# Kernel optimization log

Measured on AMD Instinct MI355X. Metric: run time of the kernel, lower is better.

Reference implementation:

```python
import jax, jax.numpy as jnp
import numpy as np

DIM = 2048
H = 16
HD = DIM // H  # 128
EPS = 1e-6


def _rmsnorm(x, w):
    # x: [b, s, d] (float32 math, matches torch RMSNorm .float())
    return x * jax.lax.rsqrt(jnp.mean(x * x, axis=-1, keepdims=True) + EPS) * w


def _rope(x, freqs):
    # x: [b, s, d]; freqs: [s, HD//2, 2] (real, imag) -- complex multiply per pair
    b, s, d = x.shape
    xp = x.reshape(b, s, H, HD // 2, 2)
    xr, xi = xp[..., 0], xp[..., 1]
    fr = freqs[None, :, None, :, 0]
    fi = freqs[None, :, None, :, 1]
    out = jnp.stack([xr * fr - xi * fi, xr * fi + xi * fr], axis=-1)
    return out.reshape(b, s, d)


def _attn(q, k, v):
    # q: [b, sq, d], k/v: [b, skv, d] -> standard SDPA over H heads
    b, sq, d = q.shape
    skv = k.shape[1]
    qh = q.reshape(b, sq, H, HD)
    kh = k.reshape(b, skv, H, HD)
    vh = v.reshape(b, skv, H, HD)
    scores = jnp.einsum('bqhd,bkhd->bhqk', qh, kh) / np.sqrt(HD).astype(np.float32)
    p = jax.nn.softmax(scores, axis=-1)
    out = jnp.einsum('bhqk,bkhd->bqhd', p, vh)
    return out.reshape(b, sq, d)


def _linear(x, w, bias):
    # torch Linear convention: w [out, in]
    return jnp.einsum('bsi,oi->bso', x, w) + bias


def setup_inputs() -> dict:
    key = jax.random.key(0)
    ks = jax.random.split(key, 24)
    rn = lambda k, sh, s=1.0: jax.random.normal(k, sh, dtype=jnp.float32) * s
    B, SX, SC, SR = 2, 2048, 512, 512
    W = 0.02
    return {
        'x': rn(ks[0], (B, SX, DIM)),
        'cam_emb': rn(ks[1], (B, SC, DIM)),
        'render_emb': rn(ks[2], (B, SR, DIM)),
        'freqs_x': rn(ks[3], (SX, HD // 2, 2)),
        'freqs_cam': rn(ks[4], (SC, HD // 2, 2)),
        'freqs_render': rn(ks[5], (SR, HD // 2, 2)),
        'wq': rn(ks[6], (DIM, DIM), W), 'bq': jnp.zeros((DIM,), jnp.float32),
        'wk': rn(ks[7], (DIM, DIM), W), 'bk': jnp.zeros((DIM,), jnp.float32),
        'wv': rn(ks[8], (DIM, DIM), W), 'bv': jnp.zeros((DIM,), jnp.float32),
        'wkr': rn(ks[9], (DIM, DIM), W), 'bkr': jnp.zeros((DIM,), jnp.float32),
        'wvr': rn(ks[10], (DIM, DIM), W), 'bvr': jnp.zeros((DIM,), jnp.float32),
        'wo': rn(ks[11], (DIM, DIM), W), 'bo': jnp.zeros((DIM,), jnp.float32),
        'gq': jnp.ones((DIM,), jnp.float32),
        'gk': jnp.ones((DIM,), jnp.float32),
    }


def reference(x, cam_emb, render_emb, freqs_x, freqs_cam, freqs_render,
              wq, bq, wk, bk, wv, bv, wkr, bkr, wvr, bvr, wo, bo, gq, gk):
    q = _rope(_rmsnorm(_linear(x, wq, bq), gq), freqs_x)
    k_cam = _rope(_rmsnorm(_linear(cam_emb, wk, bk), gk), freqs_cam)
    k_ren = _rope(_rmsnorm(_linear(render_emb, wkr, bkr), gk), freqs_render)
    v_cam = _linear(cam_emb, wv, bv)
    v_ren = _linear(render_emb, wvr, bvr)
    k = jnp.concatenate([k_cam, k_ren], axis=1)
    v = jnp.concatenate([v_cam, v_ren], axis=1)
    out = _attn(q, k, v)
    return _linear(out, wo, bo)
```

## Files before the change

kernel.cpp:

```cpp
#include <hip/hip_runtime.h>

typedef short bf16x8 __attribute__((ext_vector_type(8)));
typedef float f32x4 __attribute__((ext_vector_type(4)));
typedef unsigned short ushort_t;
typedef unsigned int uint_t;

#define DIM 2048
#define NH 16
#define HD 128

__device__ __forceinline__ ushort_t f2b(float f) {
    union { float f; uint_t u; } a; a.f = f;
    uint_t u = a.u;
    return (ushort_t)((u + 0x7fffu + ((u >> 16) & 1u)) >> 16);
}

__device__ __forceinline__ float b2f(ushort_t s) {
    union { uint_t u; float f; } a; a.u = ((uint_t)s) << 16;
    return a.f;
}

__device__ __forceinline__ uint_t cvt_pk_bf16(float lo, float hi) {
    uint_t r;
    asm("v_cvt_pk_bf16_f32 %0, %1, %2" : "=v"(r) : "v"(lo), "v"(hi));
    return r;
}

__device__ __forceinline__ void gload_lds16(const void* g, void* l) {
    void* gg = const_cast<void*>(g);
    __builtin_amdgcn_global_load_lds(
        (__attribute__((address_space(1))) uint_t*)gg,
        (__attribute__((address_space(3))) uint_t*)l, 16, 0, 0);
}

struct CvtWArgs { const float* s[6]; };
__global__ __launch_bounds__(256) void k_cvtw(CvtWArgs a, ushort_t* __restrict__ dst) {
    int y = blockIdx.y;
    const float* in = a.s[y];
    ushort_t* out = dst + (size_t)y * 4194304;
    int idx = (blockIdx.x * 256 + threadIdx.x) * 8;
    float4 p = *(const float4*)(in + idx);
    float4 q = *(const float4*)(in + idx + 4);
    uint4 o;
    o.x = (uint_t)f2b(p.x) | ((uint_t)f2b(p.y) << 16);
    o.y = (uint_t)f2b(p.z) | ((uint_t)f2b(p.w) << 16);
    o.z = (uint_t)f2b(q.x) | ((uint_t)f2b(q.y) << 16);
    o.w = (uint_t)f2b(q.z) | ((uint_t)f2b(q.w) << 16);
    *(uint4*)(out + idx) = o;
}

struct Cvt3Args { const float* s[3]; ushort_t* d[3]; int n[3]; };
__global__ __launch_bounds__(256) void k_cvt3(Cvt3Args a) {
    int y = blockIdx.y;
    int idx = (blockIdx.x * 256 + threadIdx.x) * 8;
    if (idx >= a.n[y]) return;
    const float* in = a.s[y];
    ushort_t* out = a.d[y];
    float4 p = *(const float4*)(in + idx);
    float4 q = *(const float4*)(in + idx + 4);
    uint4 o;
    o.x = (uint_t)f2b(p.x) | ((uint_t)f2b(p.y) << 16);
    o.y = (uint_t)f2b(p.z) | ((uint_t)f2b(p.w) << 16);
    o.z = (uint_t)f2b(q.x) | ((uint_t)f2b(q.y) << 16);
    o.w = (uint_t)f2b(q.z) | ((uint_t)f2b(q.w) << 16);
    *(uint4*)(out + idx) = o;
}

struct G8 {
    const ushort_t* A;
    const ushort_t* B;
    const float* bias0;
    const float* bias1;
    void* out0;
    void* out1;
};

__global__ __launch_bounds__(512, 2) void k_g256(G8 p0, G8 p1, G8 p2) {
    extern __shared__ __align__(16) char sm[];
    int tid = threadIdx.x, lane = tid & 63, w = tid >> 6;
    int c = lane & 15, g = lane >> 4;
    int wr = w >> 2, wc = w & 3;

    int flat = blockIdx.x;
    G8 ar;
    int bm, bn, isKV = 0, kvoff = 0;
    {
        int re = (flat & 7) * 32 + (flat >> 3);
        if (re < 128) { ar = p0; bm = re & 15; bn = re >> 4; }
        else {
            int r2 = re - 128;
            int z = r2 >> 6; r2 &= 63;
            ar = z ? p2 : p1;
            bm = r2 & 3; bn = r2 >> 2;
            isKV = 1; kvoff = z ? 512 : 0;
        }
    }

    int wj0 = 2 * w, wj1 = 2 * w + 1;
    int l3 = lane >> 3;
    int swz = ((lane & 7) ^ l3) << 4;
    int RA0 = (wj0 >> 3) * 128 + (wj0 & 7) * 8 + l3;
    int RA1 = (wj1 >> 3) * 128 + (wj1 & 7) * 8 + l3;
    int LB0 = wj0 * 8 + l3;
    int LB1 = wj1 * 8 + l3;
    int RB0 = (LB0 >> 5) * 64 + (LB0 & 15) * 2 + ((LB0 >> 4) & 1);
    int RB1 = (LB1 >> 5) * 64 + (LB1 & 15) * 2 + ((LB1 >> 4) & 1);
    const char* sA0 = (const char*)ar.A + (size_t)(bm * 256 + RA0) * 4096 + swz;
    const char* sA1 = (const char*)ar.A + (size_t)(bm * 256 + RA1) * 4096 + swz;
    const char* sB0 = (const char*)ar.B + (size_t)(bn * 256 + RB0) * 4096 + swz;
    const char* sB1 = (const char*)ar.B + (size_t)(bn * 256 + RB1) * 4096 + swz;
    char* dA0 = sm + wj0 * 1024;
    char* dA1 = sm + wj1 * 1024;
    char* dB0 = sm + 32768 + wj0 * 1024;
    char* dB1 = sm + 32768 + wj1 * 1024;

    auto SA = [&](int buf, int half, int t) {
        gload_lds16(sA0 + (size_t)half * 262144 + t * 128, dA0 + buf + half * 16384);
        gload_lds16(sA1 + (size_t)half * 262144 + t * 128, dA1 + buf + half * 16384);
    };
    auto SB = [&](int buf, int half, int t) {
        gload_lds16(sB0 + (size_t)half * 131072 + t * 128, dB0 + buf + half * 16384);
        gload_lds16(sB1 + (size_t)half * 131072 + t * 128, dB1 + buf + half * 16384);
    };

    int bKS0 = (g << 4) ^ ((c & 7) << 4);
    int bKS1 = (64 | (g << 4)) ^ ((c & 7) << 4);
    int aoffL = wr * 8192 + c * 128;
    int boffL = 32768 + wc * 4096 + c * 128;

    f32x4 acc[8][4];
#pragma unroll
    for (int m = 0; m < 8; m++)
#pragma unroll
        for (int n = 0; n < 4; n++) acc[m][n] = (f32x4){0.f, 0.f, 0.f, 0.f};

    bf16x8 aF[4][2], bF0[2][2], bF1[2][2];

    auto RA = [&](int buf, int mh) {
#pragma unroll
        for (int m = 0; m < 4; m++) {
            aF[m][0] = *(const bf16x8*)(sm + buf + mh * 16384 + aoffL + m * 2048 + bKS0);
            aF[m][1] = *(const bf16x8*)(sm + buf + mh * 16384 + aoffL + m * 2048 + bKS1);
        }
    };
    auto RB = [&](int buf, int nh, bf16x8 (&bF)[2][2]) {
#pragma unroll
        for (int n = 0; n < 2; n++) {
            bF[n][0] = *(const bf16x8*)(sm + buf + boffL + nh * 16384 + n * 2048 + bKS0);
            bF[n][1] = *(const bf16x8*)(sm + buf + boffL + nh * 16384 + n * 2048 + bKS1);
        }
    };
    auto MF = [&](int mh, int nh, bf16x8 (&bF)[2][2]) {
        __builtin_amdgcn_s_setprio(1);
#pragma unroll
        for (int m = 0; m < 4; m++)
#pragma unroll
            for (int n = 0; n < 2; n++)
#pragma unroll
                for (int ks = 0; ks < 2; ks++)
                    acc[mh * 4 + m][nh * 2 + n] = __builtin_amdgcn_mfma_f32_16x16x32_bf16(
                        aF[m][ks], bF[n][ks], acc[mh * 4 + m][nh * 2 + n], 0, 0, 0);
        __builtin_amdgcn_s_setprio(0);
    };

    SA(0, 0, 0); SB(0, 0, 0); SA(0, 1, 0); SB(0, 1, 0);
    SA(65536, 0, 1); SB(65536, 0, 1);
    asm volatile("s_waitcnt vmcnt(8)" ::: "memory");
    __builtin_amdgcn_s_barrier();

#pragma unroll 1
    for (int i = 0; i < 16; ++i) {
        int Tb  = 2 * i + 1;
        int Ta2 = (2 * i + 2 > 31) ? 31 : 2 * i + 2;
        int Tb2 = (2 * i + 3 > 31) ? 31 : 2 * i + 3;
        RA(0, 0); RB(0, 0, bF0);
        SA(65536, 1, Tb);
        __builtin_amdgcn_s_barrier();
        MF(0, 0, bF0);
        asm volatile("s_waitcnt vmcnt(6)" ::: "memory");
        __builtin_amdgcn_s_barrier();
        RB(0, 1, bF1);
        SB(65536, 1, Tb);
        __builtin_amdgcn_s_barrier();
        MF(0, 1, bF1);
        __builtin_amdgcn_s_barrier();
        RA(0, 1);
        SA(0, 0, Ta2);
        __builtin_amdgcn_s_barrier();
        MF(1, 0, bF0);
        __builtin_amdgcn_s_barrier();
        SB(0, 0, Ta2);
        __builtin_amdgcn_s_barrier();
        MF(1, 1, bF1);
        asm volatile("s_waitcnt vmcnt(8)" ::: "memory");
        __builtin_amdgcn_s_barrier();
        RA(65536, 0); RB(65536, 0, bF0);
        SA(0, 1, Ta2);
        __builtin_amdgcn_s_barrier();
        MF(0, 0, bF0);
        asm volatile("s_waitcnt vmcnt(6)" ::: "memory");
        __builtin_amdgcn_s_barrier();
        RB(65536, 1, bF1);
        SB(0, 1, Ta2);
        __builtin_amdgcn_s_barrier();
        MF(0, 1, bF1);
        __builtin_amdgcn_s_barrier();
        RA(65536, 1);
        SA(65536, 0, Tb2);
        __builtin_amdgcn_s_barrier();
        MF(1, 0, bF0);
        __builtin_amdgcn_s_barrier();
        SB(65536, 0, Tb2);
        __builtin_amdgcn_s_barrier();
        MF(1, 1, bF1);
        asm volatile("s_waitcnt vmcnt(8)" ::: "memory");
        __builtin_amdgcn_s_barrier();
    }

    int orow0 = bm * 256 + wr * 128 + g * 4;
    int colb0 = bn * 256 + wc * 64 + c * 2;
    if (!isKV || bn < 8) {
        ushort_t* o0 = (ushort_t*)ar.out0;
#pragma unroll
        for (int nh = 0; nh < 2; nh++) {
            int colb = colb0 + nh * 32;
            float2 bv = *(const float2*)(ar.bias0 + colb);
#pragma unroll
            for (int m = 0; m < 8; m++)
#pragma unroll
                for (int q = 0; q < 4; q++) {
                    uint_t pk = cvt_pk_bf16(acc[m][nh * 2][q] + bv.x,
                                            acc[m][nh * 2 + 1][q] + bv.y);
                    *(uint_t*)(o0 + (size_t)(orow0 + m * 16 + q) * 2048 + colb) = pk;
                }
        }
    } else {
        ushort_t* o1 = (ushort_t*)ar.out1;
#pragma unroll
        for (int nh = 0; nh < 2; nh++)
#pragma unroll
            for (int np = 0; np < 2; np++) {
                int col2 = colb0 + nh * 32 + np - 2048;
                int h = col2 >> 7, d = col2 & 127;
                float bvs = ar.bias1[col2];
#pragma unroll
                for (int m = 0; m < 8; m++) {
                    int r = orow0 + m * 16;
                    int bb = r >> 9;
                    int kvg = kvoff + (r & 511);
                    int t = kvg >> 6, ki = kvg & 63;
                    uint2 wv;
                    wv.x = cvt_pk_bf16(acc[m][nh * 2 + np][0] + bvs, acc[m][nh * 2 + np][1] + bvs);
                    wv.y = cvt_pk_bf16(acc[m][nh * 2 + np][2] + bvs, acc[m][nh * 2 + np][3] + bvs);
                    *(uint2*)(o1 + (size_t)((bb * 16 + h) * 16 + t) * 8192 + d * 64 + ki) = wv;
                }
            }
    }
}

__global__ __launch_bounds__(512, 2) void k_g128(G8 p0) {
    extern __shared__ __align__(16) char sm[];
    int tid = threadIdx.x, lane = tid & 63, w = tid >> 6;
    int c = lane & 15, g = lane >> 4;
    int wr = w >> 2, wc = w & 3;

    int flat = blockIdx.x;
    int re = (flat & 7) * 32 + (flat >> 3);
    int bm = re & 31, bn = re >> 5;
    G8 ar = p0;

    int l3 = lane >> 3;
    int swz = ((lane & 7) ^ l3) << 4;
    int wj0 = 2 * w, wj1 = 2 * w + 1;
    int LB0 = wj0 * 8 + l3;
    int LB1 = wj1 * 8 + l3;
    int RB0 = (LB0 >> 5) * 64 + (LB0 & 15) * 2 + ((LB0 >> 4) & 1);
    int RB1 = (LB1 >> 5) * 64 + (LB1 & 15) * 2 + ((LB1 >> 4) & 1);
    const char* sA  = (const char*)ar.A + (size_t)(bm * 128 + w * 8 + l3) * 4096 + swz;
    const char* sB0 = (const char*)ar.B + (size_t)(bn * 256 + RB0) * 4096 + swz;
    const char* sB1 = (const char*)ar.B + (size_t)(bn * 256 + RB1) * 4096 + swz;
    char* dA  = sm + w * 1024;
    char* dB0 = sm + 16384 + wj0 * 1024;
    char* dB1 = sm + 16384 + wj1 * 1024;

    auto SA = [&](int buf, int half, int t) {
        gload_lds16(sA + (size_t)half * 262144 + t * 128, dA + buf + half * 8192);
    };
    auto SB = [&](int buf, int half, int t) {
        gload_lds16(sB0 + (size_t)half * 131072 + t * 128, dB0 + buf + half * 16384);
        gload_lds16(sB1 + (size_t)half * 131072 + t * 128, dB1 + buf + half * 16384);
    };

    int bKS0 = (g << 4) ^ ((c & 7) << 4);
    int bKS1 = (64 | (g << 4)) ^ ((c & 7) << 4);
    int aoffL = wr * 8192 + c * 128;
    int boffL = 16384 + wc * 4096 + c * 128;

    f32x4 acc[4][4];
#pragma unroll
    for (int m = 0; m < 4; m++)
#pragma unroll
        for (int n = 0; n < 4; n++) acc[m][n] = (f32x4){0.f, 0.f, 0.f, 0.f};

    bf16x8 aF[2][2], bF0[2][2], bF1[2][2];

    auto RA = [&](int buf, int mhp) {
#pragma unroll
        for (int m = 0; m < 2; m++) {
            aF[m][0] = *(const bf16x8*)(sm + buf + aoffL + (mhp * 2 + m) * 2048 + bKS0);
            aF[m][1] = *(const bf16x8*)(sm + buf + aoffL + (mhp * 2 + m) * 2048 + bKS1);
        }
    };
    auto RB = [&](int buf, int nh, bf16x8 (&bF)[2][2]) {
#pragma unroll
        for (int n = 0; n < 2; n++) {
            bF[n][0] = *(const bf16x8*)(sm + buf + boffL + nh * 16384 + n * 2048 + bKS0);
            bF[n][1] = *(const bf16x8*)(sm + buf + boffL + nh * 16384 + n * 2048 + bKS1);
        }
    };
    auto MF = [&](int mhp, int nh, bf16x8 (&bF)[2][2]) {
        __builtin_amdgcn_s_setprio(1);
#pragma unroll
        for (int m = 0; m < 2; m++)
#pragma unroll
            for (int n = 0; n < 2; n++)
#pragma unroll
                for (int ks = 0; ks < 2; ks++)
                    acc[mhp * 2 + m][nh * 2 + n] = __builtin_amdgcn_mfma_f32_16x16x32_bf16(
                        aF[m][ks], bF[n][ks], acc[mhp * 2 + m][nh * 2 + n], 0, 0, 0);
        __builtin_amdgcn_s_setprio(0);
    };

    const int B1 = 49152;
    SA(0, 0, 0); SA(0, 1, 0); SB(0, 0, 0); SB(0, 1, 0);
    SA(B1, 0, 1);
    asm volatile("s_waitcnt vmcnt(1)" ::: "memory");
    __builtin_amdgcn_s_barrier();

#pragma unroll 1
    for (int i = 0; i < 16; ++i) {
        int Tb  = 2 * i + 1;
        int Ta2 = (2 * i + 2 > 31) ? 31 : 2 * i + 2;
        int Tb2 = (2 * i + 3 > 31) ? 31 : 2 * i + 3;
        RA(0, 0); RB(0, 0, bF0);
        SA(B1, 1, Tb);
        __builtin_amdgcn_s_barrier();
        MF(0, 0, bF0);
        __builtin_amdgcn_s_barrier();
        RB(0, 1, bF1);
        SB(B1, 0, Tb);
        __builtin_amdgcn_s_barrier();
        MF(0, 1, bF1);
        __builtin_amdgcn_s_barrier();
        RA(0, 1);
        SB(B1, 1, Tb);
        __builtin_amdgcn_s_barrier();
        MF(1, 0, bF0);
        __builtin_amdgcn_s_barrier();
        SA(0, 0, Ta2);
        __builtin_amdgcn_s_barrier();
        MF(1, 1, bF1);
        asm volatile("s_waitcnt vmcnt(3)" ::: "memory");
        __builtin_amdgcn_s_barrier();
        RA(B1, 0); RB(B1, 0, bF0);
        SA(0, 1, Ta2);
        __builtin_amdgcn_s_barrier();
        MF(0, 0, bF0);
        asm volatile("s_waitcnt vmcnt(2)" ::: "memory");
        __builtin_amdgcn_s_barrier();
        RB(B1, 1, bF1);
        SB(0, 0, Ta2);
        __builtin_amdgcn_s_barrier();
        MF(0, 1, bF1);
        __builtin_amdgcn_s_barrier();
        RA(B1, 1);
        SB(0, 1, Ta2);
        __builtin_amdgcn_s_barrier();
        MF(1, 0, bF0);
        __builtin_amdgcn_s_barrier();
        SA(B1, 0, Tb2);
        __builtin_amdgcn_s_barrier();
        MF(1, 1, bF1);
        asm volatile("s_waitcnt vmcnt(1)" ::: "memory");
        __builtin_amdgcn_s_barrier();
    }

    int orow0 = bm * 128 + wr * 64 + g * 4;
    int colb0 = bn * 256 + wc * 64 + c * 2;
    float* o0 = (float*)ar.out0;
#pragma unroll
    for (int nh = 0; nh < 2; nh++) {
        int colb = colb0 + nh * 32;
        float2 bv = *(const float2*)(ar.bias0 + colb);
#pragma unroll
        for (int m = 0; m < 4; m++)
#pragma unroll
            for (int q = 0; q < 4; q++) {
                float2 st = {acc[m][nh * 2][q] + bv.x, acc[m][nh * 2 + 1][q] + bv.y};
                *(float2*)(o0 + (size_t)(orow0 + m * 16 + q) * 2048 + colb) = st;
            }
    }
}

struct RR { const ushort_t* in; const float* gain; const float* freqs; ushort_t* out; int lgS; float scale; };
__global__ __launch_bounds__(256) void k_rr(RR a0, RR a1, RR a2) {
    int bid = blockIdx.x;
    RR a; int row;
    if (bid < 4096) { a = a0; row = bid; }
    else if (bid < 5120) { a = a1; row = bid - 4096; }
    else { a = a2; row = bid - 5120; }
    int S = 1 << a.lgS;
    int s = row & (S - 1);
    int b = row >> a.lgS;
    int tid = threadIdx.x;
    uint4 v = *(const uint4*)(a.in + (size_t)row * 2048 + tid * 8);
    ushort_t us[8];
    us[0] = (ushort_t)(v.x & 0xffff); us[1] = (ushort_t)(v.x >> 16);
    us[2] = (ushort_t)(v.y & 0xffff); us[3] = (ushort_t)(v.y >> 16);
    us[4] = (ushort_t)(v.z & 0xffff); us[5] = (ushort_t)(v.z >> 16);
    us[6] = (ushort_t)(v.w & 0xffff); us[7] = (ushort_t)(v.w >> 16);
    float y[8];
#pragma unroll
    for (int j = 0; j < 8; j++) y[j] = b2f(us[j]);
    float ss = 0.f;
#pragma unroll
    for (int j = 0; j < 8; j++) ss += y[j] * y[j];
#pragma unroll
    for (int off = 32; off > 0; off >>= 1) ss += __shfl_xor(ss, off, 64);
    __shared__ float red[4];
    int lane = tid & 63, wid = tid >> 6;
    if (lane == 0) red[wid] = ss;
    __syncthreads();
    float tot = red[0] + red[1] + red[2] + red[3];
    float inv = rsqrtf(tot * (1.0f / DIM) + 1e-6f);
    const float* gp = a.gain + tid * 8;
    float4 g0 = *(const float4*)gp;
    float4 g1 = *(const float4*)(gp + 4);
    float gg[8] = {g0.x, g0.y, g0.z, g0.w, g1.x, g1.y, g1.z, g1.w};
    int p0 = (tid * 8 & 127) >> 1;
    const float* fq = a.freqs + ((size_t)s * 64 + p0) * 2;
    uint_t ow[4];
#pragma unroll
    for (int j = 0; j < 4; j++) {
        float fr = fq[j * 2 + 0], fi = fq[j * 2 + 1];
        float xr = y[2 * j] * inv * gg[2 * j];
        float xi = y[2 * j + 1] * inv * gg[2 * j + 1];
        float o0 = (xr * fr - xi * fi) * a.scale;
        float o1 = (xr * fi + xi * fr) * a.scale;
        ow[j] = (uint_t)f2b(o0) | ((uint_t)f2b(o1) << 16);
    }
    int h = tid >> 4;
    ushort_t* dst = a.out + ((size_t)((b * 16 + h) * S + s)) * 128 + (tid & 15) * 8;
    *(uint4*)dst = make_uint4(ow[0], ow[1], ow[2], ow[3]);
}

__global__ __launch_bounds__(512, 4) void k_attn(const ushort_t* __restrict__ Q,
                                                 const ushort_t* __restrict__ Kc,
                                                 const ushort_t* __restrict__ Kr,
                                                 const ushort_t* __restrict__ Vt,
                                                 ushort_t* __restrict__ O) {
    __shared__ __align__(16) char sm[65536];
    int tid = threadIdx.x, lane = tid & 63, w = tid >> 6;
    int c = lane & 15, g = lane >> 4;

    int bid = blockIdx.x;
    int xcd = bid & 7, idx = bid >> 3;
    int combo = idx & 3, qt = idx >> 2;
    int b = combo >> 1, h = xcd * 2 + (combo & 1);
    int bh = b * 16 + h;

    const ushort_t* qg = Q + ((size_t)(bh * 2048 + qt * 128 + w * 16 + c)) * 128 + g * 8;
    bf16x8 aQ[4];
#pragma unroll
    for (int ks = 0; ks < 4; ks++) aQ[ks] = *(const bf16x8*)(qg + ks * 32);

    int kbase[4], vbase[8];
#pragma unroll
    for (int n = 0; n < 4; n++) {
        int row = ((n >> 1) << 5) + ((c >> 2) << 3) + ((n & 1) << 2) + (c & 3);
        int sw = (row & 3) | (((row >> 3) & 3) << 2);
        kbase[n] = row * 256 + ((g ^ sw) << 4);
    }
#pragma unroll
    for (int dt = 0; dt < 8; dt++) {
        int vrow = dt * 16 + c;
        vbase[dt] = vrow * 128 + ((g ^ (vrow & 7)) << 4);
    }

    int swk = (lane >> 4) | ((w & 3) << 2);
    int klo = (8 * w + (lane >> 4)) * 256 + (((lane & 15) ^ swk) << 4);
    int vlo = (16 * w + (lane >> 3)) * 128 + (((lane & 7) ^ (lane >> 3)) << 4);
    int dst0 = w * 2048;

    const char* kcb = (const char*)Kc + (size_t)bh * 131072;
    const char* krb = (const char*)Kr + (size_t)bh * 131072;
    const char* vtb = (const char*)Vt + (size_t)bh * 262144;

    float mr = -1e30f, lr = 0.f;
    f32x4 o[8];
#pragma unroll
    for (int d = 0; d < 8; d++) o[d] = (f32x4){0, 0, 0, 0};

    auto STAGE = [&](int DB, int t) {
        const char* kg = (t < 8) ? kcb + t * 16384 : krb + (t - 8) * 16384;
        const char* vg = vtb + t * 16384;
        gload_lds16(kg + klo, sm + DB + dst0);
        gload_lds16(kg + klo + 1024, sm + DB + dst0 + 1024);
        gload_lds16(vg + vlo, sm + DB + 16384 + dst0);
        gload_lds16(vg + vlo + 1024, sm + DB + 16384 + dst0 + 1024);
    };

    auto TILE = [&](int DB) {
        f32x4 sT[4];
#pragma unroll
        for (int n = 0; n < 4; n++) sT[n] = (f32x4){0, 0, 0, 0};
#pragma unroll
        for (int n = 0; n < 4; n++)
#pragma unroll
            for (int ks = 0; ks < 4; ks++) {
                bf16x8 aK = *(const bf16x8*)(sm + DB + (kbase[n] ^ (ks << 6)));
                sT[n] = __builtin_amdgcn_mfma_f32_16x16x32_bf16(aK, aQ[ks], sT[n], 0, 0, 0);
            }
        float mloc = sT[0][0];
#pragma unroll
        for (int n = 0; n < 4; n++)
#pragma unroll
            for (int r = 0; r < 4; r++) mloc = fmaxf(mloc, sT[n][r]);
        if (!__all(mloc - mr <= 8.0f)) {
            float mx = fmaxf(mloc, __shfl_xor(mloc, 16, 64));
            mx = fmaxf(mx, __shfl_xor(mx, 32, 64));
            float mn = fmaxf(mr, mx);
            float al = exp2f(mr - mn);
            mr = mn;
            lr *= al;
#pragma unroll
            for (int d = 0; d < 8; d++) o[d] *= al;
        }
        float p[4][4];
        float ps = 0.f;
#pragma unroll
        for (int n = 0; n < 4; n++)
#pragma unroll
            for (int r = 0; r < 4; r++) {
                p[n][r] = exp2f(sT[n][r] - mr);
                ps += p[n][r];
            }
        lr += ps;
#pragma unroll
        for (int kk = 0; kk < 2; kk++) {
            union { uint_t u[4]; bf16x8 v; } bP;
            bP.u[0] = cvt_pk_bf16(p[2 * kk][0], p[2 * kk][1]);
            bP.u[1] = cvt_pk_bf16(p[2 * kk][2], p[2 * kk][3]);
            bP.u[2] = cvt_pk_bf16(p[2 * kk + 1][0], p[2 * kk + 1][1]);
            bP.u[3] = cvt_pk_bf16(p[2 * kk + 1][2], p[2 * kk + 1][3]);
#pragma unroll
            for (int dt = 0; dt < 8; dt++) {
                bf16x8 aV = *(const bf16x8*)(sm + DB + 16384 + (vbase[dt] ^ (kk << 6)));
                o[dt] = __builtin_amdgcn_mfma_f32_16x16x32_bf16(aV, bP.v, o[dt], 0, 0, 0);
            }
        }
    };

    STAGE(0, 0);
    __syncthreads();
#pragma unroll 1
    for (int t = 0; t < 16; t += 2) {
        STAGE(32768, t + 1);
        TILE(0);
        __syncthreads();
        if (t < 14) STAGE(0, t + 2);
        TILE(32768);
        __syncthreads();
    }

    lr += __shfl_xor(lr, 16, 64);
    lr += __shfl_xor(lr, 32, 64);
    float inv = 1.0f / lr;
    ushort_t* lO = (ushort_t*)sm;
#pragma unroll
    for (int dt = 0; dt < 8; dt++) {
        uint2 wv;
        wv.x = (uint_t)f2b(o[dt][0] * inv) | ((uint_t)f2b(o[dt][1] * inv) << 16);
        wv.y = (uint_t)f2b(o[dt][2] * inv) | ((uint_t)f2b(o[dt][3] * inv) << 16);
        *(uint2*)(lO + (w * 16 + c) * 136 + dt * 16 + g * 4) = wv;
    }
    __syncthreads();
    int row = tid >> 2, c8 = tid & 3;
    const ushort_t* src = lO + row * 136 + c8 * 32;
    ushort_t* dst = O + (size_t)(b * 2048 + qt * 128 + row) * 2048 + h * 128 + c8 * 32;
#pragma unroll
    for (int k = 0; k < 4; k++) *(uint4*)(dst + k * 8) = *(const uint4*)(src + k * 8);
}

extern "C" void kernel_launch(void* const* d_in, const int* in_sizes, int n_in,
                              void* d_out, int out_size, void* d_ws, size_t ws_size,
                              hipStream_t stream) {
    const float* x   = (const float*)d_in[0];
    const float* cam = (const float*)d_in[1];
    const float* ren = (const float*)d_in[2];
    const float* fx  = (const float*)d_in[3];
    const float* fc  = (const float*)d_in[4];
    const float* fr  = (const float*)d_in[5];
    const float* wq  = (const float*)d_in[6];
    const float* bq  = (const float*)d_in[7];
    const float* wk  = (const float*)d_in[8];
    const float* bk  = (const float*)d_in[9];
    const float* wv  = (const float*)d_in[10];
    const float* bv  = (const float*)d_in[11];
    const float* wkr = (const float*)d_in[12];
    const float* bkr = (const float*)d_in[13];
    const float* wvr = (const float*)d_in[14];
    const float* bvr = (const float*)d_in[15];
    const float* wo  = (const float*)d_in[16];
    const float* bo  = (const float*)d_in[17];
    const float* gq  = (const float*)d_in[18];
    const float* gk  = (const float*)d_in[19];

    char* ws = (char*)d_ws;
    ushort_t* wq_b     = (ushort_t*)(ws + 0);
    ushort_t* wk_b     = (ushort_t*)(ws + 8388608);
    ushort_t* wkr_b    = (ushort_t*)(ws + 25165824);
    ushort_t* wo_b     = (ushort_t*)(ws + 41943040);
    ushort_t* xb       = (ushort_t*)(ws + 50331648);
    ushort_t* camb     = (ushort_t*)(ws + 67108864);
    ushort_t* renb     = (ushort_t*)(ws + 71303168);
    ushort_t* kcam_lin = (ushort_t*)(ws + 75497472);
    ushort_t* kren_lin = (ushort_t*)(ws + 79691776);
    ushort_t* vt       = (ushort_t*)(ws + 83886080);
    ushort_t* q_bf     = (ushort_t*)(ws + 92274688);
    ushort_t* kcam_bf  = (ushort_t*)(ws + 109051904);
    ushort_t* kren_bf  = (ushort_t*)(ws + 113246208);
    ushort_t* attn_bf  = (ushort_t*)(ws + 50331648);
    ushort_t* q_lin    = (ushort_t*)d_out;

    hipFuncSetAttribute(reinterpret_cast<const void*>(&k_g256),
                        hipFuncAttributeMaxDynamicSharedMemorySize, 131072);
    hipFuncSetAttribute(reinterpret_cast<const void*>(&k_g128),
                        hipFuncAttributeMaxDynamicSharedMemorySize, 98304);

    CvtWArgs cw{{wq, wk, wv, wkr, wvr, wo}};
    k_cvtw<<<dim3(2048, 6), 256, 0, stream>>>(cw, wq_b);
    Cvt3Args c3{{x, cam, ren}, {xb, camb, renb}, {8388608, 2097152, 2097152}};
    k_cvt3<<<dim3(4096, 3), 256, 0, stream>>>(c3);

    G8 qa{xb, wq_b, bq, nullptr, (void*)q_lin, nullptr};
    G8 kva0{camb, wk_b, bk, bv, (void*)kcam_lin, (void*)vt};
    G8 kva1{renb, wkr_b, bkr, bvr, (void*)kren_lin, (void*)vt};
    k_g256<<<dim3(256, 1, 1), 512, 131072, stream>>>(qa, kva0, kva1);

    RR r0{q_lin, gq, fx, q_bf, 11, 0.08838834764831845f * 1.4426950408889634f};
    RR r1{kcam_lin, gk, fc, kcam_bf, 9, 1.0f};
    RR r2{kren_lin, gk, fr, kren_bf, 9, 1.0f};
    k_rr<<<dim3(6144, 1, 1), 256, 0, stream>>>(r0, r1, r2);

    k_attn<<<dim3(512, 1, 1), 512, 0, stream>>>(q_bf, kcam_bf, kren_bf, vt, attn_bf);

    G8 oa{attn_bf, wo_b, bo, nullptr, d_out, nullptr};
    k_g128<<<dim3(256, 1, 1), 512, 98304, stream>>>(oa);
}
```

Measured before the change: 207.9 us.

## Use 16-wave blocks in projection GEMM and merge conversion kernels

The fused QKV projection GEMM now runs with 1024 threads (16 waves) per block instead of 512. Each wave owns a 64x64 output tile with half the accumulators, and the prefetch/barrier schedule is simpler, with full vmcnt(0) waits per half-step. The weight and activation fp32-to-bf16 conversions are merged into one grid-stride kernel launch. The change trades the old fine-grained overlap of loads with MFMA for more waves to hide latency, but the full drains may expose load latency.

```diff
diff --git a/kernel.cpp b/kernel.cpp
--- a/kernel.cpp
+++ b/kernel.cpp
@@ -33,37 +33,22 @@
         (__attribute__((address_space(3))) uint_t*)l, 16, 0, 0);
 }
 
-struct CvtWArgs { const float* s[6]; };
-__global__ __launch_bounds__(256) void k_cvtw(CvtWArgs a, ushort_t* __restrict__ dst) {
+struct Cvt9 { const float* s[9]; ushort_t* d[9]; int n[9]; };
+__global__ __launch_bounds__(256) void k_cvt9(Cvt9 a) {
     int y = blockIdx.y;
     const float* in = a.s[y];
-    ushort_t* out = dst + (size_t)y * 4194304;
-    int idx = (blockIdx.x * 256 + threadIdx.x) * 8;
-    float4 p = *(const float4*)(in + idx);
-    float4 q = *(const float4*)(in + idx + 4);
-    uint4 o;
-    o.x = (uint_t)f2b(p.x) | ((uint_t)f2b(p.y) << 16);
-    o.y = (uint_t)f2b(p.z) | ((uint_t)f2b(p.w) << 16);
-    o.z = (uint_t)f2b(q.x) | ((uint_t)f2b(q.y) << 16);
-    o.w = (uint_t)f2b(q.z) | ((uint_t)f2b(q.w) << 16);
-    *(uint4*)(out + idx) = o;
-}
-
-struct Cvt3Args { const float* s[3]; ushort_t* d[3]; int n[3]; };
-__global__ __launch_bounds__(256) void k_cvt3(Cvt3Args a) {
-    int y = blockIdx.y;
-    int idx = (blockIdx.x * 256 + threadIdx.x) * 8;
-    if (idx >= a.n[y]) return;
-    const float* in = a.s[y];
     ushort_t* out = a.d[y];
-    float4 p = *(const float4*)(in + idx);
-    float4 q = *(const float4*)(in + idx + 4);
-    uint4 o;
-    o.x = (uint_t)f2b(p.x) | ((uint_t)f2b(p.y) << 16);
-    o.y = (uint_t)f2b(p.z) | ((uint_t)f2b(p.w) << 16);
-    o.z = (uint_t)f2b(q.x) | ((uint_t)f2b(q.y) << 16);
-    o.w = (uint_t)f2b(q.z) | ((uint_t)f2b(q.w) << 16);
-    *(uint4*)(out + idx) = o;
+    int n = a.n[y];
+    for (int idx = (blockIdx.x * 256 + threadIdx.x) * 8; idx < n; idx += 2048 * 256 * 8) {
+        float4 p = *(const float4*)(in + idx);
+        float4 q = *(const float4*)(in + idx + 4);
+        uint4 o;
+        o.x = (uint_t)f2b(p.x) | ((uint_t)f2b(p.y) << 16);
+        o.y = (uint_t)f2b(p.z) | ((uint_t)f2b(p.w) << 16);
+        o.z = (uint_t)f2b(q.x) | ((uint_t)f2b(q.y) << 16);
+        o.w = (uint_t)f2b(q.z) | ((uint_t)f2b(q.w) << 16);
+        *(uint4*)(out + idx) = o;
+    }
 }
 
 struct G8 {
@@ -75,7 +60,7 @@
     void* out1;
 };
 
-__global__ __launch_bounds__(512, 2) void k_g256(G8 p0, G8 p1, G8 p2) {
+__global__ __launch_bounds__(1024, 1) void k_g256(G8 p0, G8 p1, G8 p2) {
     extern __shared__ __align__(16) char sm[];
     int tid = threadIdx.x, lane = tid & 63, w = tid >> 6;
     int c = lane & 15, g = lane >> 4;
@@ -96,128 +81,109 @@
         }
     }
 
-    int wj0 = 2 * w, wj1 = 2 * w + 1;
+    int row_local = tid >> 3;
     int l3 = lane >> 3;
     int swz = ((lane & 7) ^ l3) << 4;
-    int RA0 = (wj0 >> 3) * 128 + (wj0 & 7) * 8 + l3;
-    int RA1 = (wj1 >> 3) * 128 + (wj1 & 7) * 8 + l3;
-    int LB0 = wj0 * 8 + l3;
-    int LB1 = wj1 * 8 + l3;
-    int RB0 = (LB0 >> 5) * 64 + (LB0 & 15) * 2 + ((LB0 >> 4) & 1);
-    int RB1 = (LB1 >> 5) * 64 + (LB1 & 15) * 2 + ((LB1 >> 4) & 1);
-    const char* sA0 = (const char*)ar.A + (size_t)(bm * 256 + RA0) * 4096 + swz;
-    const char* sA1 = (const char*)ar.A + (size_t)(bm * 256 + RA1) * 4096 + swz;
-    const char* sB0 = (const char*)ar.B + (size_t)(bn * 256 + RB0) * 4096 + swz;
-    const char* sB1 = (const char*)ar.B + (size_t)(bn * 256 + RB1) * 4096 + swz;
-    char* dA0 = sm + wj0 * 1024;
-    char* dA1 = sm + wj1 * 1024;
-    char* dB0 = sm + 32768 + wj0 * 1024;
-    char* dB1 = sm + 32768 + wj1 * 1024;
-
-    auto SA = [&](int buf, int half, int t) {
-        gload_lds16(sA0 + (size_t)half * 262144 + t * 128, dA0 + buf + half * 16384);
-        gload_lds16(sA1 + (size_t)half * 262144 + t * 128, dA1 + buf + half * 16384);
-    };
-    auto SB = [&](int buf, int half, int t) {
-        gload_lds16(sB0 + (size_t)half * 131072 + t * 128, dB0 + buf + half * 16384);
-        gload_lds16(sB1 + (size_t)half * 131072 + t * 128, dB1 + buf + half * 16384);
+    const char* srcA[2];
+#pragma unroll
+    for (int h = 0; h < 2; h++)
+        srcA[h] = (const char*)ar.A + (size_t)(bm * 256 + h * 128 + row_local) * 4096 + swz;
+    const char* srcB[2];
+#pragma unroll
+    for (int h = 0; h < 2; h++) {
+        int x = h * 128 + row_local;
+        int grp = x >> 5, j = x & 31;
+        int gr = grp * 32 + (j & 15) * 2 + (j >> 4);
+        srcB[h] = (const char*)ar.B + (size_t)(bn * 256 + gr) * 4096 + swz;
+    }
+    char* dstW = sm + w * 1024;
+
+    auto SAh = [&](int buf, int h, int t) {
+        gload_lds16(srcA[h] + (size_t)t * 128, dstW + buf + h * 16384);
+    };
+    auto SBh = [&](int buf, int h, int t) {
+        gload_lds16(srcB[h] + (size_t)t * 128, dstW + buf + 32768 + h * 16384);
     };
 
     int bKS0 = (g << 4) ^ ((c & 7) << 4);
     int bKS1 = (64 | (g << 4)) ^ ((c & 7) << 4);
-    int aoffL = wr * 8192 + c * 128;
-    int boffL = 32768 + wc * 4096 + c * 128;
-
-    f32x4 acc[8][4];
-#pragma unroll
-    for (int m = 0; m < 8; m++)
+    int aBase = (wr >> 1) * 16384 + ((wr & 1) * 64 + c) * 128;
+    int bBase = 32768 + (wc >> 1) * 16384 + ((wc & 1) * 64 + c) * 128;
+
+    f32x4 acc[4][4];
+#pragma unroll
+    for (int m = 0; m < 4; m++)
 #pragma unroll
         for (int n = 0; n < 4; n++) acc[m][n] = (f32x4){0.f, 0.f, 0.f, 0.f};
 
-    bf16x8 aF[4][2], bF0[2][2], bF1[2][2];
-
-    auto RA = [&](int buf, int mh) {
-#pragma unroll
-        for (int m = 0; m < 4; m++) {
-            aF[m][0] = *(const bf16x8*)(sm + buf + mh * 16384 + aoffL + m * 2048 + bKS0);
-            aF[m][1] = *(const bf16x8*)(sm + buf + mh * 16384 + aoffL + m * 2048 + bKS1);
-        }
-    };
-    auto RB = [&](int buf, int nh, bf16x8 (&bF)[2][2]) {
-#pragma unroll
-        for (int n = 0; n < 2; n++) {
-            bF[n][0] = *(const bf16x8*)(sm + buf + boffL + nh * 16384 + n * 2048 + bKS0);
-            bF[n][1] = *(const bf16x8*)(sm + buf + boffL + nh * 16384 + n * 2048 + bKS1);
-        }
-    };
-    auto MF = [&](int mh, int nh, bf16x8 (&bF)[2][2]) {
+    const int B1 = 65536;
+
+    auto PH_START = [&](int buf, int nh, bf16x8 (&a0)[4], bf16x8 (&b0v)[2]) {
+#pragma unroll
+        for (int m = 0; m < 4; m++)
+            a0[m] = *(const bf16x8*)(sm + buf + aBase + m * 2048 + bKS0);
+#pragma unroll
+        for (int n2 = 0; n2 < 2; n2++)
+            b0v[n2] = *(const bf16x8*)(sm + buf + bBase + (nh * 2 + n2) * 2048 + bKS0);
+    };
+    auto PH_END = [&](int buf, int nh, bf16x8 (&a0)[4], bf16x8 (&b0v)[2]) {
         __builtin_amdgcn_s_setprio(1);
 #pragma unroll
         for (int m = 0; m < 4; m++)
 #pragma unroll
-            for (int n = 0; n < 2; n++)
-#pragma unroll
-                for (int ks = 0; ks < 2; ks++)
-                    acc[mh * 4 + m][nh * 2 + n] = __builtin_amdgcn_mfma_f32_16x16x32_bf16(
-                        aF[m][ks], bF[n][ks], acc[mh * 4 + m][nh * 2 + n], 0, 0, 0);
+            for (int n2 = 0; n2 < 2; n2++)
+                acc[m][nh * 2 + n2] = __builtin_amdgcn_mfma_f32_16x16x32_bf16(
+                    a0[m], b0v[n2], acc[m][nh * 2 + n2], 0, 0, 0);
+        bf16x8 a1[4], b1v[2];
+#pragma unroll
+        for (int m = 0; m < 4; m++)
+            a1[m] = *(const bf16x8*)(sm + buf + aBase + m * 2048 + bKS1);
+#pragma unroll
+        for (int n2 = 0; n2 < 2; n2++)
+            b1v[n2] = *(const bf16x8*)(sm + buf + bBase + (nh * 2 + n2) * 2048 + bKS1);
+#pragma unroll
+        for (int m = 0; m < 4; m++)
+#pragma unroll
+            for (int n2 = 0; n2 < 2; n2++)
+                acc[m][nh * 2 + n2] = __builtin_amdgcn_mfma_f32_16x16x32_bf16(
+                    a1[m], b1v[n2], acc[m][nh * 2 + n2], 0, 0, 0);
         __builtin_amdgcn_s_setprio(0);
     };
 
-    SA(0, 0, 0); SB(0, 0, 0); SA(0, 1, 0); SB(0, 1, 0);
-    SA(65536, 0, 1); SB(65536, 0, 1);
-    asm volatile("s_waitcnt vmcnt(8)" ::: "memory");
+    SAh(0, 0, 0); SAh(0, 1, 0); SBh(0, 0, 0); SBh(0, 1, 0);
+    asm volatile("s_waitcnt vmcnt(0)" ::: "memory");
     __builtin_amdgcn_s_barrier();
 
 #pragma unroll 1
     for (int i = 0; i < 16; ++i) {
         int Tb  = 2 * i + 1;
         int Ta2 = (2 * i + 2 > 31) ? 31 : 2 * i + 2;
-        int Tb2 = (2 * i + 3 > 31) ? 31 : 2 * i + 3;
-        RA(0, 0); RB(0, 0, bF0);
-        SA(65536, 1, Tb);
-        __builtin_amdgcn_s_barrier();
-        MF(0, 0, bF0);
-        asm volatile("s_waitcnt vmcnt(6)" ::: "memory");
-        __builtin_amdgcn_s_barrier();
-        RB(0, 1, bF1);
-        SB(65536, 1, Tb);
-        __builtin_amdgcn_s_barrier();
-        MF(0, 1, bF1);
-        __builtin_amdgcn_s_barrier();
-        RA(0, 1);
-        SA(0, 0, Ta2);
-        __builtin_amdgcn_s_barrier();
-        MF(1, 0, bF0);
-        __builtin_amdgcn_s_barrier();
-        SB(0, 0, Ta2);
-        __builtin_amdgcn_s_barrier();
-        MF(1, 1, bF1);
-        asm volatile("s_waitcnt vmcnt(8)" ::: "memory");
-        __builtin_amdgcn_s_barrier();
-        RA(65536, 0); RB(65536, 0, bF0);
-        SA(0, 1, Ta2);
-        __builtin_amdgcn_s_barrier();
-        MF(0, 0, bF0);
-        asm volatile("s_waitcnt vmcnt(6)" ::: "memory");
-        __builtin_amdgcn_s_barrier();
-        RB(65536, 1, bF1);
-        SB(0, 1, Ta2);
-        __builtin_amdgcn_s_barrier();
-        MF(0, 1, bF1);
-        __builtin_amdgcn_s_barrier();
-        RA(65536, 1);
-        SA(65536, 0, Tb2);
-        __builtin_amdgcn_s_barrier();
-        MF(1, 0, bF0);
-        __builtin_amdgcn_s_barrier();
-        SB(65536, 0, Tb2);
-        __builtin_amdgcn_s_barrier();
-        MF(1, 1, bF1);
-        asm volatile("s_waitcnt vmcnt(8)" ::: "memory");
-        __builtin_amdgcn_s_barrier();
-    }
-
-    int orow0 = bm * 256 + wr * 128 + g * 4;
+        bf16x8 aF[4], bF[2];
+        SAh(B1, 0, Tb); SAh(B1, 1, Tb);
+        PH_START(0, 0, aF, bF);
+        __builtin_amdgcn_s_barrier();
+        PH_END(0, 0, aF, bF);
+        __builtin_amdgcn_s_barrier();
+        SBh(B1, 0, Tb); SBh(B1, 1, Tb);
+        PH_START(0, 1, aF, bF);
+        __builtin_amdgcn_s_barrier();
+        PH_END(0, 1, aF, bF);
+        asm volatile("s_waitcnt vmcnt(0)" ::: "memory");
+        __builtin_amdgcn_s_barrier();
+        SAh(0, 0, Ta2); SAh(0, 1, Ta2);
+        PH_START(B1, 0, aF, bF);
+        __builtin_amdgcn_s_barrier();
+        PH_END(B1, 0, aF, bF);
+        __builtin_amdgcn_s_barrier();
+        SBh(0, 0, Ta2); SBh(0, 1, Ta2);
+        PH_START(B1, 1, aF, bF);
+        __builtin_amdgcn_s_barrier();
+        PH_END(B1, 1, aF, bF);
+        asm volatile("s_waitcnt vmcnt(0)" ::: "memory");
+        __builtin_amdgcn_s_barrier();
+    }
+
+    int orow0 = bm * 256 + wr * 64 + g * 4;
     int colb0 = bn * 256 + wc * 64 + c * 2;
     if (!isKV || bn < 8) {
         ushort_t* o0 = (ushort_t*)ar.out0;
@@ -226,7 +192,7 @@
             int colb = colb0 + nh * 32;
             float2 bv = *(const float2*)(ar.bias0 + colb);
 #pragma unroll
-            for (int m = 0; m < 8; m++)
+            for (int m = 0; m < 4; m++)
 #pragma unroll
                 for (int q = 0; q < 4; q++) {
                     uint_t pk = cvt_pk_bf16(acc[m][nh * 2][q] + bv.x,
@@ -244,7 +210,7 @@
                 int h = col2 >> 7, d = col2 & 127;
                 float bvs = ar.bias1[col2];
 #pragma unroll
-                for (int m = 0; m < 8; m++) {
+                for (int m = 0; m < 4; m++) {
                     int r = orow0 + m * 16;
                     int bb = r >> 9;
                     int kvg = kvoff + (r & 511);
@@ -638,15 +604,24 @@
     hipFuncSetAttribute(reinterpret_cast<const void*>(&k_g128),
                         hipFuncAttributeMaxDynamicSharedMemorySize, 98304);
 
-    CvtWArgs cw{{wq, wk, wv, wkr, wvr, wo}};
-    k_cvtw<<<dim3(2048, 6), 256, 0, stream>>>(cw, wq_b);
-    Cvt3Args c3{{x, cam, ren}, {xb, camb, renb}, {8388608, 2097152, 2097152}};
-    k_cvt3<<<dim3(4096, 3), 256, 0, stream>>>(c3);
+    ushort_t* wv_b  = wk_b + 4194304;
+    ushort_t* wvr_b = wkr_b + 4194304;
+    Cvt9 c9;
+    c9.s[0] = wq;  c9.d[0] = wq_b;  c9.n[0] = 4194304;
+    c9.s[1] = wk;  c9.d[1] = wk_b;  c9.n[1] = 4194304;
+    c9.s[2] = wv;  c9.d[2] = wv_b;  c9.n[2] = 4194304;
+    c9.s[3] = wkr; c9.d[3] = wkr_b; c9.n[3] = 4194304;
+    c9.s[4] = wvr; c9.d[4] = wvr_b; c9.n[4] = 4194304;
+    c9.s[5] = wo;  c9.d[5] = wo_b;  c9.n[5] = 4194304;
+    c9.s[6] = x;   c9.d[6] = xb;    c9.n[6] = 8388608;
+    c9.s[7] = cam; c9.d[7] = camb;  c9.n[7] = 2097152;
+    c9.s[8] = ren; c9.d[8] = renb;  c9.n[8] = 2097152;
+    k_cvt9<<<dim3(2048, 9), 256, 0, stream>>>(c9);
 
     G8 qa{xb, wq_b, bq, nullptr, (void*)q_lin, nullptr};
     G8 kva0{camb, wk_b, bk, bv, (void*)kcam_lin, (void*)vt};
     G8 kva1{renb, wkr_b, bkr, bvr, (void*)kren_lin, (void*)vt};
-    k_g256<<<dim3(256, 1, 1), 512, 131072, stream>>>(qa, kva0, kva1);
+    k_g256<<<dim3(256, 1, 1), 1024, 131072, stream>>>(qa, kva0, kva1);
 
     RR r0{q_lin, gq, fx, q_bf, 11, 0.08838834764831845f * 1.4426950408889634f};
     RR r1{kcam_lin, gk, fc, kcam_bf, 9, 1.0f};
```

Measured after the change: 211.3 us. About the same (+1.6%).
